# Performance work log

Hardware: AMD Instinct MI355X
Metric: run time of the kernel (lower is better)

The kernel has to match this reference:

```python
import jax, jax.numpy as jnp
import numpy as np

N_NODES = 10000
N_EDGES = 640000
D_FEAT = 128
N_CLASSES = 40


def setup_inputs() -> dict:
    key = jax.random.key(0)
    k1, k2, k3, k4 = jax.random.split(key, 4)
    x = jax.random.normal(k1, (N_NODES, D_FEAT), dtype=jnp.float32)
    edge_index = jax.random.randint(k2, (2, N_EDGES), 0, N_NODES, dtype=jnp.int64)
    # SAGEConv params: lin_l (neighbor path, with bias), lin_r (root path, no bias)
    W_l = jax.random.normal(k3, (D_FEAT, N_CLASSES), dtype=jnp.float32) / np.sqrt(D_FEAT)
    b_l = jnp.zeros((N_CLASSES,), dtype=jnp.float32)
    W_r = jax.random.normal(k4, (D_FEAT, N_CLASSES), dtype=jnp.float32) / np.sqrt(D_FEAT)
    return {"x": x, "edge_index": edge_index, "W_l": W_l, "b_l": b_l, "W_r": W_r}


def reference(x, edge_index, W_l, b_l, W_r):
    # SAGEConv(aggr='max'): gather source features, scatter-max into destinations
    src, dst = edge_index[0], edge_index[1]
    msgs = x[src]                                        # [E, F] gather
    agg = jax.ops.segment_max(msgs, dst, num_segments=x.shape[0])  # [N, F]
    # nodes with no incoming edges: PyG fills with 0
    agg = jnp.where(jnp.isneginf(agg), 0.0, agg)
    out = agg @ W_l + b_l + x @ W_r                      # [N, C]
    return jax.nn.log_softmax(out, axis=1)
```

## Files before the change

kernel.cpp:

```cpp
#include <hip/hip_runtime.h>
#include <math.h>

#define D_FEAT 128
#define N_CLASSES 40
#define CAP 128

#define CNT_PAD_INTS (10000 * 16)
#define XH_BYTES (10000 * D_FEAT * 2)
#define CNT_BYTES (CNT_PAD_INTS * 4)
#define WPK_U32 (64 * N_CLASSES)

typedef int v4i __attribute__((ext_vector_type(4)));
typedef _Float16 h2 __attribute__((ext_vector_type(2)));

static __device__ __forceinline__ unsigned int pkmax(unsigned int a, unsigned int b) {
    unsigned int d;
    asm("v_pk_max_f16 %0, %1, %2" : "=v"(d) : "v"(a), "v"(b));
    return d;
}
static __device__ __forceinline__ float fdot2(unsigned int a, unsigned int b, float c) {
    return __builtin_amdgcn_fdot2(__builtin_bit_cast(h2, a),
                                  __builtin_bit_cast(h2, b), c, false);
}
static __device__ __forceinline__ unsigned short f2h(float f) {
    return __builtin_bit_cast(unsigned short, (_Float16)f);
}


extern "C" __global__ void __launch_bounds__(256)
gnn_cvt(const float* __restrict__ x, unsigned int* __restrict__ xh,
        int* __restrict__ cnt,
        const float* __restrict__ W_l, const float* __restrict__ W_r,
        unsigned int* __restrict__ Wlpk, unsigned int* __restrict__ Wrpk, int n4)
{
    int t = blockIdx.x * 256 + threadIdx.x;
    if (t < CNT_PAD_INTS / 4) {
        reinterpret_cast<v4i*>(cnt)[t] = (v4i){0, 0, 0, 0};
    }
    if (t < WPK_U32) {
        int f2 = t / N_CLASSES, c = t % N_CLASSES;
        Wlpk[t] = (unsigned int)f2h(W_l[(2 * f2) * N_CLASSES + c])
                | ((unsigned int)f2h(W_l[(2 * f2 + 1) * N_CLASSES + c]) << 16);
        Wrpk[t] = (unsigned int)f2h(W_r[(2 * f2) * N_CLASSES + c])
                | ((unsigned int)f2h(W_r[(2 * f2 + 1) * N_CLASSES + c]) << 16);
    }
    if (t >= n4) return;
    float4 v = reinterpret_cast<const float4*>(x)[t];
    uint2 o;
    o.x = (unsigned int)f2h(v.x) | ((unsigned int)f2h(v.y) << 16);
    o.y = (unsigned int)f2h(v.z) | ((unsigned int)f2h(v.w) << 16);
    reinterpret_cast<uint2*>(xh)[t] = o;
}

extern "C" __global__ void __launch_bounds__(256)
gnn_bucketize(const int* __restrict__ src, const int* __restrict__ dst,
              int* __restrict__ cnt, unsigned short* __restrict__ bucket,
              int n_edges4)
{
    int t = blockIdx.x * 256 + threadIdx.x;
    if (t >= n_edges4) return;
    v4i s4 = __builtin_nontemporal_load(reinterpret_cast<const v4i*>(src) + t);
    v4i d4 = __builtin_nontemporal_load(reinterpret_cast<const v4i*>(dst) + t);
    int p0 = atomicAdd(&cnt[d4.x << 4], 1);
    int p1 = atomicAdd(&cnt[d4.y << 4], 1);
    int p2 = atomicAdd(&cnt[d4.z << 4], 1);
    int p3 = atomicAdd(&cnt[d4.w << 4], 1);
    if (p0 < CAP) bucket[(size_t)d4.x * CAP + p0] = (unsigned short)s4.x;
    if (p1 < CAP) bucket[(size_t)d4.y * CAP + p1] = (unsigned short)s4.y;
    if (p2 < CAP) bucket[(size_t)d4.z * CAP + p2] = (unsigned short)s4.z;
    if (p3 < CAP) bucket[(size_t)d4.w * CAP + p3] = (unsigned short)s4.w;
}

extern "C" __global__ void __launch_bounds__(256)
gnn_fused(const unsigned int* __restrict__ xh,
          const int* __restrict__ cnt, const unsigned short* __restrict__ bucket,
          const unsigned int* __restrict__ Wlpk, const unsigned int* __restrict__ Wrpk,
          const float* __restrict__ b_l,
          float* __restrict__ out, int n_nodes)
{
    __shared__ unsigned int sa2[4][64];
    __shared__ unsigned int sx2[4][64];

    const int wave = threadIdx.x >> 6;
    const int lane = threadIdx.x & 63;
    const int node = blockIdx.x * 4 + wave;
    const bool valid = (node < n_nodes);

    const int sub = lane >> 4;
    const int q   = lane & 15;

    int deg = 0;
    if (valid) deg = min(cnt[node << 4], CAP);

    unsigned int acc2[4];
    #pragma unroll
    for (int i = 0; i < 4; ++i) acc2[i] = 0xFC00FC00u;

    const unsigned short* brow = bucket + (size_t)node * CAP;
    const uint4* xh4 = reinterpret_cast<const uint4*>(xh);

    for (int base = 0; base < deg; base += 64) {
        const int nb = min(64, deg - base);
        int myid = brow[base + min(lane, nb - 1)];

        if (nb == 64) {
            #pragma unroll
            for (int k = 0; k < 64; k += 16) {
                int ss[4];
                #pragma unroll
                for (int j = 0; j < 4; ++j) ss[j] = __shfl(myid, k + 4 * j + sub, 64);
                uint4 vv[4];
                #pragma unroll
                for (int j = 0; j < 4; ++j) vv[j] = xh4[ss[j] * 16 + q];
                #pragma unroll
                for (int j = 0; j < 4; ++j) {
                    const unsigned int* u = &vv[j].x;
                    #pragma unroll
                    for (int w = 0; w < 4; ++w) acc2[w] = pkmax(acc2[w], u[w]);
                }
            }
        } else {
            for (int k = 0; k < nb; k += 8) {
                int e0 = min(k + sub, nb - 1);
                int e1 = min(k + 4 + sub, nb - 1);
                int s0 = __shfl(myid, e0, 64);
                int s1 = __shfl(myid, e1, 64);
                uint4 v0 = xh4[s0 * 16 + q];
                uint4 v1 = xh4[s1 * 16 + q];
                const unsigned int* u0 = &v0.x;
                const unsigned int* u1 = &v1.x;
                #pragma unroll
                for (int w = 0; w < 4; ++w) {
                    acc2[w] = pkmax(acc2[w], u0[w]);
                    acc2[w] = pkmax(acc2[w], u1[w]);
                }
            }
        }
    }

    #pragma unroll
    for (int i = 0; i < 4; ++i) {
        acc2[i] = pkmax(acc2[i], (unsigned int)__shfl_xor((int)acc2[i], 16, 64));
        acc2[i] = pkmax(acc2[i], (unsigned int)__shfl_xor((int)acc2[i], 32, 64));
    }
    if (deg == 0) {
        #pragma unroll
        for (int i = 0; i < 4; ++i) acc2[i] = 0u;
    }

    if (valid) {
        if (sub == 0) {
            uint4 w4;
            w4.x = acc2[0]; w4.y = acc2[1]; w4.z = acc2[2]; w4.w = acc2[3];
            *reinterpret_cast<uint4*>(&sa2[wave][q * 4]) = w4;
        }
        if (lane < 16) {
            reinterpret_cast<uint4*>(sx2[wave])[lane] = xh4[node * 16 + lane];
        }
    }

    float o = 0.0f;
    if (valid && lane < N_CLASSES) {
        o = b_l[lane];
        const uint4* a4 = reinterpret_cast<const uint4*>(sa2[wave]);
        const uint4* x4 = reinterpret_cast<const uint4*>(sx2[wave]);
        #pragma unroll 4
        for (int i = 0; i < 16; ++i) {
            uint4 a  = a4[i];
            uint4 xx = x4[i];
            const unsigned int* ua = &a.x;
            const unsigned int* ux = &xx.x;
            #pragma unroll
            for (int j = 0; j < 4; ++j) {
                int f2 = i * 4 + j;
                o = fdot2(ua[j], Wlpk[f2 * N_CLASSES + lane], o);
                o = fdot2(ux[j], Wrpk[f2 * N_CLASSES + lane], o);
            }
        }
    }

    float mm = (valid && lane < N_CLASSES) ? o : -INFINITY;
    #pragma unroll
    for (int off = 32; off > 0; off >>= 1) mm = fmaxf(mm, __shfl_xor(mm, off, 64));
    float ex = (valid && lane < N_CLASSES) ? expf(o - mm) : 0.0f;
    float ss = ex;
    #pragma unroll
    for (int off = 32; off > 0; off >>= 1) ss += __shfl_xor(ss, off, 64);

    if (valid && lane < N_CLASSES)
        out[(size_t)node * N_CLASSES + lane] = o - mm - logf(ss);
}

extern "C" void kernel_launch(void* const* d_in, const int* in_sizes, int n_in,
                              void* d_out, int out_size, void* d_ws, size_t ws_size,
                              hipStream_t stream) {
    const float* x   = (const float*)d_in[0];
    const int*   ei  = (const int*)d_in[1];
    const float* W_l = (const float*)d_in[2];
    const float* b_l = (const float*)d_in[3];
    const float* W_r = (const float*)d_in[4];
    float* out = (float*)d_out;

    const int n_nodes = in_sizes[0] / D_FEAT;
    const int n_edges = in_sizes[1] / 2;
    const int* src = ei;
    const int* dst = ei + n_edges;

    char* w = (char*)d_ws;
    unsigned int* xh = (unsigned int*)w;
    int* cnt = (int*)(w + XH_BYTES);
    unsigned int* Wlpk = (unsigned int*)(w + XH_BYTES + CNT_BYTES);
    unsigned int* Wrpk = Wlpk + WPK_U32;
    unsigned short* bucket = (unsigned short*)(w + XH_BYTES + CNT_BYTES
                                               + 2 * WPK_U32 * 4);

    {
        int n4 = n_nodes * D_FEAT / 4;
        int blocks = (n4 + 255) / 256;
        gnn_cvt<<<blocks, 256, 0, stream>>>(x, xh, cnt, W_l, W_r, Wlpk, Wrpk, n4);
    }
    {
        int n_edges4 = n_edges / 4;
        int blocks = (n_edges4 + 255) / 256;
        gnn_bucketize<<<blocks, 256, 0, stream>>>(src, dst, cnt, bucket, n_edges4);
    }
    {
        int blocks = (n_nodes + 3) / 4;
        gnn_fused<<<blocks, 256, 0, stream>>>(xh, cnt, bucket, Wlpk, Wrpk, b_l,
                                              out, n_nodes);
    }
}
```

Measured before the change: 59.93 us.

## Partition bucketize atomics by destination range per XCD and deepen gather batching

The bucketize kernel is launched with eight times as many blocks. Consecutive blocks (block index mod 8) each handle only the destination nodes in one eighth of the node range, so each edge chunk is read eight times. The intent is that blocks landing on the same XCD touch a disjoint slice of the count and bucket arrays, keeping atomics and scattered writes local to that XCD's L2. The fused kernel's full-chunk gather now issues 8 loads per batch instead of 4 to raise memory-level parallelism, at the cost of more registers. The trade-off is eightfold index reads and a dependence on round-robin block-to-XCD placement, with NODES_PER_XCD hardcoded for 10000 nodes.

```diff
diff --git a/kernel.cpp b/kernel.cpp
--- a/kernel.cpp
+++ b/kernel.cpp
@@ -4,9 +4,12 @@
 #define D_FEAT 128
 #define N_CLASSES 40
 #define CAP 128
-
-#define CNT_PAD_INTS (10000 * 16)
-#define XH_BYTES (10000 * D_FEAT * 2)
+#define N_NODES_C 10000
+#define NXCD 8
+#define NODES_PER_XCD (N_NODES_C / NXCD)
+
+#define CNT_PAD_INTS (N_NODES_C * 16)
+#define XH_BYTES (N_NODES_C * D_FEAT * 2)
 #define CNT_BYTES (CNT_PAD_INTS * 4)
 #define WPK_U32 (64 * N_CLASSES)
 
@@ -57,18 +60,24 @@
               int* __restrict__ cnt, unsigned short* __restrict__ bucket,
               int n_edges4)
 {
-    int t = blockIdx.x * 256 + threadIdx.x;
+    const int r  = blockIdx.x & (NXCD - 1);
+    const int t  = (blockIdx.x >> 3) * 256 + threadIdx.x;
     if (t >= n_edges4) return;
-    v4i s4 = __builtin_nontemporal_load(reinterpret_cast<const v4i*>(src) + t);
-    v4i d4 = __builtin_nontemporal_load(reinterpret_cast<const v4i*>(dst) + t);
-    int p0 = atomicAdd(&cnt[d4.x << 4], 1);
-    int p1 = atomicAdd(&cnt[d4.y << 4], 1);
-    int p2 = atomicAdd(&cnt[d4.z << 4], 1);
-    int p3 = atomicAdd(&cnt[d4.w << 4], 1);
-    if (p0 < CAP) bucket[(size_t)d4.x * CAP + p0] = (unsigned short)s4.x;
-    if (p1 < CAP) bucket[(size_t)d4.y * CAP + p1] = (unsigned short)s4.y;
-    if (p2 < CAP) bucket[(size_t)d4.z * CAP + p2] = (unsigned short)s4.z;
-    if (p3 < CAP) bucket[(size_t)d4.w * CAP + p3] = (unsigned short)s4.w;
+    const int lo = r * NODES_PER_XCD;
+    const int hi = lo + NODES_PER_XCD;
+
+    v4i s4 = reinterpret_cast<const v4i*>(src)[t];
+    v4i d4 = reinterpret_cast<const v4i*>(dst)[t];
+
+    #pragma unroll
+    for (int j = 0; j < 4; ++j) {
+        int d = (j == 0) ? d4.x : (j == 1) ? d4.y : (j == 2) ? d4.z : d4.w;
+        int s = (j == 0) ? s4.x : (j == 1) ? s4.y : (j == 2) ? s4.z : s4.w;
+        if (d >= lo && d < hi) {
+            int p = atomicAdd(&cnt[d << 4], 1);
+            if (p < CAP) bucket[(size_t)d * CAP + p] = (unsigned short)s;
+        }
+    }
 }
 
 extern "C" __global__ void __launch_bounds__(256)
@@ -105,15 +114,15 @@
 
         if (nb == 64) {
             #pragma unroll
-            for (int k = 0; k < 64; k += 16) {
-                int ss[4];
-                #pragma unroll
-                for (int j = 0; j < 4; ++j) ss[j] = __shfl(myid, k + 4 * j + sub, 64);
-                uint4 vv[4];
-                #pragma unroll
-                for (int j = 0; j < 4; ++j) vv[j] = xh4[ss[j] * 16 + q];
-                #pragma unroll
-                for (int j = 0; j < 4; ++j) {
+            for (int k = 0; k < 64; k += 32) {
+                int ss[8];
+                #pragma unroll
+                for (int j = 0; j < 8; ++j) ss[j] = __shfl(myid, k + 4 * j + sub, 64);
+                uint4 vv[8];
+                #pragma unroll
+                for (int j = 0; j < 8; ++j) vv[j] = xh4[ss[j] * 16 + q];
+                #pragma unroll
+                for (int j = 0; j < 8; ++j) {
                     const unsigned int* u = &vv[j].x;
                     #pragma unroll
                     for (int w = 0; w < 4; ++w) acc2[w] = pkmax(acc2[w], u[w]);
@@ -221,8 +230,9 @@
     }
     {
         int n_edges4 = n_edges / 4;
-        int blocks = (n_edges4 + 255) / 256;
-        gnn_bucketize<<<blocks, 256, 0, stream>>>(src, dst, cnt, bucket, n_edges4);
+        int chunks = (n_edges4 + 255) / 256;
+        gnn_bucketize<<<chunks * NXCD, 256, 0, stream>>>(src, dst, cnt, bucket,
+                                                         n_edges4);
     }
     {
         int blocks = (n_nodes + 3) / 4;
```

Result: no change. 60.77 us (+1.4%).
